# Optimization experiments

Measured on AMD Instinct MI355X. Metric: run time of the kernel, lower is better.

Reference implementation:

```python
import jax, jax.numpy as jnp
import numpy as np

WS = (7, 7)  # window size
NUM_HEADS = 16


def _relative_position_index(ws):
    # Deterministic int index table, computed exactly as in the torch module.
    coords = np.stack(np.meshgrid(np.arange(ws[0]), np.arange(ws[1]), indexing='ij'))  # [2,Wh,Ww]
    coords = coords.reshape(2, -1)                       # [2, N]
    rel = coords[:, :, None] - coords[:, None, :]        # [2, N, N]
    rel = rel.transpose(1, 2, 0)                         # [N, N, 2]
    rel = rel + np.array([ws[0] - 1, ws[1] - 1])
    rel[:, :, 0] *= 2 * ws[1] - 1
    return jnp.asarray(rel.sum(-1), dtype=jnp.int32)     # [N, N]


def setup_inputs() -> dict:
    key = jax.random.key(0)
    ks = jax.random.split(key, 5)
    B_, N, C = 2048, WS[0] * WS[1], 512
    nw = 64
    return {
        'x': jax.random.normal(ks[0], (B_, N, C), dtype=jnp.float32),
        'mask': jax.random.normal(ks[1], (nw, N, N), dtype=jnp.float32),
        'qkv_w': jax.random.normal(ks[2], (3 * C, C), dtype=jnp.float32) * 0.02,
        'qkv_b': jax.random.normal(ks[3], (3 * C,), dtype=jnp.float32) * 0.02,
        'rpb_table': jax.random.normal(ks[4], ((2 * WS[0] - 1) * (2 * WS[1] - 1), NUM_HEADS), dtype=jnp.float32) * 0.02,
    }


def reference(x, mask, qkv_w, qkv_b, rpb_table):
    B_, N, C = x.shape
    H = NUM_HEADS
    hd = C // H
    scale = hd ** -0.5

    # qkv projection: [B_, N, 3, H, hd] -> q, k, v each [B_, H, N, hd]
    qkv = (jnp.einsum('bnc,oc->bno', x, qkv_w) + qkv_b)
    qkv = qkv.reshape(B_, N, 3, H, hd).transpose(2, 0, 3, 1, 4)
    q, k, v = qkv[0], qkv[1], qkv[2]

    attn = jnp.einsum('bhnd,bhmd->bhnm', q * scale, k)  # [B_, H, N, N]

    rel_idx = _relative_position_index(WS)                       # [N, N]
    bias = rpb_table[rel_idx.reshape(-1)].reshape(N, N, H)       # gather
    attn = attn + bias.transpose(2, 0, 1)[None]                  # [1, H, N, N]

    nw = mask.shape[0]
    attn = attn.reshape(B_ // nw, nw, H, N, N) + mask[None, :, None]
    attn = attn.reshape(B_, H, N, N)
    attn = jax.nn.softmax(attn, axis=-1)

    out = jnp.einsum('bhnm,bhmd->bhnd', attn, v)
    out = out.transpose(0, 2, 1, 3).reshape(B_, N, C)
    # NOTE: source assigns `X = self.proj(x)` but returns `x`, so the
    # output projection is dead code; we faithfully return pre-proj output.
    return out
```

## Files before the change

kernel.cpp:

```cpp
#include <hip/hip_runtime.h>
#include <cstdint>
#include <cstddef>

typedef __bf16 bf16x8 __attribute__((ext_vector_type(8)));
typedef float f32x4 __attribute__((ext_vector_type(4)));
typedef unsigned short u16x8 __attribute__((ext_vector_type(8)));
typedef unsigned short u16x4 __attribute__((ext_vector_type(4)));
typedef unsigned int u32x2 __attribute__((ext_vector_type(2)));

#define VT_LD 56
#define BSTRIDE 52
#define BSZ 2548
#define PLD 72

__device__ __forceinline__ unsigned short f2bf(float f) {
  unsigned int u = __builtin_bit_cast(unsigned int, f);
  u += 0x7FFFu + ((u >> 16) & 1u);
  return (unsigned short)(u >> 16);
}
__device__ __forceinline__ float bf2f(unsigned short h) {
  unsigned int u = (unsigned int)h << 16;
  return __builtin_bit_cast(float, u);
}

__device__ __forceinline__ void gload_lds16(const void* g, void* l) {
  __builtin_amdgcn_global_load_lds((const __attribute__((address_space(1))) void*)g,
                                   (__attribute__((address_space(3))) void*)l, 16, 0, 0);
}

__global__ void conv_f2b_k(const float* __restrict__ src, unsigned short* __restrict__ dst, long n8) {
  long i = (long)blockIdx.x * blockDim.x + threadIdx.x;
  long stride = (long)gridDim.x * blockDim.x;
  for (; i < n8; i += stride) {
    float4 a = *(const float4*)(src + i * 8);
    float4 b = *(const float4*)(src + i * 8 + 4);
    u16x8 p;
    p[0]=f2bf(a.x); p[1]=f2bf(a.y); p[2]=f2bf(a.z); p[3]=f2bf(a.w);
    p[4]=f2bf(b.x); p[5]=f2bf(b.y); p[6]=f2bf(b.z); p[7]=f2bf(b.w);
    *(u16x8*)(dst + i * 8) = p;
  }
}

__global__ void build_bias_k(const float* __restrict__ rpb, unsigned short* __restrict__ biasT) {
  int idx = blockIdx.x * 256 + threadIdx.x;
  if (idx >= 16 * BSZ) return;
  int h = idx / BSZ;
  int rem = idx - h * BSZ;
  int i = rem / BSTRIDE, j = rem - (rem / BSTRIDE) * BSTRIDE;
  unsigned short v = 0;
  if (j < 49) {
    int r1 = i / 7, c1 = i - r1 * 7;
    int r2 = j / 7, c2 = j - r2 * 7;
    int ri = (r1 - r2 + 6) * 13 + (c1 - c2 + 6);
    v = f2bf(rpb[ri * 16 + h]);
  }
  biasT[idx] = v;
}

#define GEMM_SETUP(N0)                                                         \
  int t = threadIdx.x;                                                         \
  int lane = t & 63, wv = t >> 6;                                              \
  int g = lane >> 4, q = lane & 15;                                            \
  int wrow = wv >> 1, wcol = wv & 1;                                           \
  f32x4 acc[4][4] = {};                                                        \
  int schunk = (t & 3) ^ ((t >> 3) & 3);                                       \
  const unsigned short* ag0 = xb + (m0 + (t >> 2)) * 512 + schunk * 8;         \
  const unsigned short* ag1 = ag0 + 64 * 512;                                  \
  const unsigned short* bg0 = wb + (size_t)((N0) + (t >> 2)) * 512 + schunk * 8; \
  const unsigned short* bg1 = bg0 + 64 * 512;                                  \
  unsigned short* alA  = Ab + wv * 512;                                        \
  unsigned short* alA2 = Ab + 2048 + wv * 512;                                 \
  unsigned short* blB  = Bb + wv * 512;                                        \
  unsigned short* blB2 = Bb + 2048 + wv * 512;                                 \
  int roff = (8 * g) ^ (((q >> 1) & 3) << 3);                                  \
  const unsigned short* arb = Ab + (wrow * 64 + q) * 32 + roff;                \
  const unsigned short* brb = Bb + (wcol * 64 + q) * 32 + roff;

#define STAGE(KT, BOFF) do {                    \
    int kof = (KT) * 32;                        \
    gload_lds16(ag0 + kof, alA  + (BOFF));      \
    gload_lds16(ag1 + kof, alA2 + (BOFF));      \
    gload_lds16(bg0 + kof, blB  + (BOFF));      \
    gload_lds16(bg1 + kof, blB2 + (BOFF));      \
  } while (0)

#define COMPUTE(BOFF, SWAPPED) do {                                            \
    bf16x8 af[4], bfr[4];                                                      \
    _Pragma("unroll")                                                          \
    for (int i2 = 0; i2 < 4; ++i2) af[i2]  = *(const bf16x8*)(arb + (BOFF) + i2 * 512); \
    _Pragma("unroll")                                                          \
    for (int j2 = 0; j2 < 4; ++j2) bfr[j2] = *(const bf16x8*)(brb + (BOFF) + j2 * 512); \
    _Pragma("unroll")                                                          \
    for (int i2 = 0; i2 < 4; ++i2)                                             \
      _Pragma("unroll")                                                        \
      for (int j2 = 0; j2 < 4; ++j2)                                           \
        acc[i2][j2] = (SWAPPED)                                                \
          ? __builtin_amdgcn_mfma_f32_16x16x32_bf16(bfr[j2], af[i2], acc[i2][j2], 0, 0, 0) \
          : __builtin_amdgcn_mfma_f32_16x16x32_bf16(af[i2], bfr[j2], acc[i2][j2], 0, 0, 0); \
  } while (0)

#define KLOOP(SWAPPED)                          \
  STAGE(0, 0);                                  \
  __syncthreads();                              \
  for (int kt = 0; kt < 16; kt += 2) {          \
    STAGE(kt + 1, 4096);                        \
    COMPUTE(0, SWAPPED);                        \
    __syncthreads();                            \
    if (kt + 2 < 16) STAGE(kt + 2, 0);          \
    COMPUTE(4096, SWAPPED);                     \
    __syncthreads();                            \
  }

__global__ __launch_bounds__(256, 4) void qkv_gemm_qk_k(
    const unsigned short* __restrict__ xb, const float* __restrict__ qkv_b,
    const unsigned short* __restrict__ wb,
    unsigned short* __restrict__ qs, unsigned short* __restrict__ kk)
{
  __shared__ __align__(16) unsigned short smem[16384];
  unsigned short* Ab = smem;
  unsigned short* Bb = smem + 8192;

  int bid = blockIdx.x;
  int sw = (bid & 7) * 784 + (bid >> 3);
  int mt = sw >> 3, ntl = sw & 7;
  long m0 = (long)mt * 128;
  int  n0 = ntl * 128;
  int  s  = n0 >> 9;

  GEMM_SETUP(n0)
  KLOOP(1)

  unsigned short* dst = (s == 0) ? qs : kk;
  float sc = (s == 0) ? 0.17677669529663687f : 1.0f;
  float4 bi[4];
  int hj[4], dj[4];
  #pragma unroll
  for (int j2 = 0; j2 < 4; ++j2) {
    int n = n0 + wcol * 64 + j2 * 16 + 4 * g;
    bi[j2] = *(const float4*)(qkv_b + n);
    hj[j2] = (n >> 5) & 15;
    dj[j2] = n & 31;
  }
  #pragma unroll
  for (int i2 = 0; i2 < 4; ++i2) {
    unsigned int m = (unsigned int)m0 + wrow * 64 + i2 * 16 + q;
    unsigned int b = m / 49;
    unsigned int i = m - b * 49;
    size_t base = ((size_t)(b * 16) * 49 + i) * 32;
    #pragma unroll
    for (int j2 = 0; j2 < 4; ++j2) {
      f32x4 a = acc[i2][j2];
      unsigned int lo = (unsigned int)f2bf((a[0] + bi[j2].x) * sc) | ((unsigned int)f2bf((a[1] + bi[j2].y) * sc) << 16);
      unsigned int hi = (unsigned int)f2bf((a[2] + bi[j2].z) * sc) | ((unsigned int)f2bf((a[3] + bi[j2].w) * sc) << 16);
      u32x2 wv2 = {lo, hi};
      *(u32x2*)(dst + base + (size_t)hj[j2] * (49 * 32) + dj[j2]) = wv2;
    }
  }
}

__global__ __launch_bounds__(256, 4) void qkv_gemm_v_k(
    const unsigned short* __restrict__ xb, const float* __restrict__ qkv_b,
    const unsigned short* __restrict__ wb,
    unsigned short* __restrict__ vt)
{
  __shared__ __align__(16) unsigned short smem[16384];
  unsigned short* Ab = smem;
  unsigned short* Bb = smem + 8192;

  int bid = blockIdx.x;
  int sw = (bid & 7) * 392 + (bid >> 3);
  int mt = sw >> 2, ntv = sw & 3;
  long m0 = (long)mt * 128;
  int  n0 = 1024 + ntv * 128;

  GEMM_SETUP(n0)
  KLOOP(0)

  #pragma unroll
  for (int j2 = 0; j2 < 4; ++j2) {
    int n  = n0 + wcol * 64 + j2 * 16 + q;
    float bias = qkv_b[n];
    int d = n & 31;
    int h = (n >> 5) & 15;
    #pragma unroll
    for (int i2 = 0; i2 < 4; ++i2) {
      unsigned int gm0 = (unsigned int)m0 + wrow * 64 + i2 * 16 + 4 * g;
      unsigned int b0 = gm0 / 49;
      unsigned int i0 = gm0 - b0 * 49;
      unsigned short hv[4];
      #pragma unroll
      for (int r = 0; r < 4; ++r) hv[r] = f2bf(acc[i2][j2][r] + bias);
      if (i0 <= 45) {
        unsigned short* base = vt + ((size_t)(b0 * 16 + h) * 32 + d) * VT_LD;
        if ((i0 & 1) == 0) {
          *(unsigned int*)(base + i0)     = (unsigned int)hv[0] | ((unsigned int)hv[1] << 16);
          *(unsigned int*)(base + i0 + 2) = (unsigned int)hv[2] | ((unsigned int)hv[3] << 16);
        } else {
          base[i0] = hv[0];
          *(unsigned int*)(base + i0 + 1) = (unsigned int)hv[1] | ((unsigned int)hv[2] << 16);
          base[i0 + 3] = hv[3];
        }
      } else {
        #pragma unroll
        for (int r = 0; r < 4; ++r) {
          unsigned int gm = gm0 + r;
          unsigned int b = gm / 49;
          unsigned int i = gm - b * 49;
          vt[((size_t)(b * 16 + h) * 32 + d) * VT_LD + i] = hv[r];
        }
      }
    }
  }
}

__global__ __launch_bounds__(256, 3) void win_attn_k(
    const unsigned short* __restrict__ qs, const unsigned short* __restrict__ kk,
    const unsigned short* __restrict__ vt, const unsigned short* __restrict__ biasT,
    const float* __restrict__ mask, float* __restrict__ out)
{
  __shared__ float mlds[BSZ];
  __shared__ unsigned short plds[4][64 * PLD];

  int b = blockIdx.x;
  int t = threadIdx.x;
  int lane = t & 63, wv = t >> 6;
  int g = lane >> 4, q = lane & 15;

  const float* msrc = mask + (size_t)(b & 63) * 2401;
  for (int idx = t; idx < BSZ; idx += 256) {
    int i = idx / BSTRIDE, j = idx - (idx / BSTRIDE) * BSTRIDE;
    mlds[idx] = (j < 49) ? msrc[i * 49 + j] : 0.0f;
  }
  __syncthreads();

  unsigned short* pl = plds[wv];
  const float NINF = -__builtin_inff();

  int rc[4];
  rc[0] = q; rc[1] = 16 + q; rc[2] = 32 + q; rc[3] = 48;

  int h0 = wv * 4;
  const unsigned short* qh = qs + (size_t)(b * 16 + h0) * (49 * 32);
  const unsigned short* kh = kk + (size_t)(b * 16 + h0) * (49 * 32);
  bf16x8 ak[4], bq[4];
  #pragma unroll
  for (int jt = 0; jt < 4; ++jt) ak[jt] = *(const bf16x8*)(kh + rc[jt] * 32 + 8 * g);
  #pragma unroll
  for (int it = 0; it < 4; ++it) bq[it] = *(const bf16x8*)(qh + rc[it] * 32 + 8 * g);

  #pragma unroll
  for (int hh = 0; hh < 4; ++hh) {
    int h = wv * 4 + hh;
    const unsigned short* vh  = vt + (size_t)(b * 16 + h) * (32 * VT_LD);
    const unsigned short* bh2 = biasT + h * BSZ;

    f32x4 zero = {0.f, 0.f, 0.f, 0.f};
    f32x4 st[4][4];
    __builtin_amdgcn_s_setprio(1);
    #pragma unroll
    for (int it = 0; it < 4; ++it)
      #pragma unroll
      for (int jt = 0; jt < 4; ++jt)
        st[it][jt] = __builtin_amdgcn_mfma_f32_16x16x32_bf16(ak[jt], bq[it], zero, 0, 0, 0);
    __builtin_amdgcn_s_setprio(0);

    bf16x8 akn[4], bqn[4];
    if (hh < 3) {
      const unsigned short* qh2 = qh + 49 * 32;
      const unsigned short* kh2 = kh + 49 * 32;
      #pragma unroll
      for (int jt = 0; jt < 4; ++jt) akn[jt] = *(const bf16x8*)(kh2 + rc[jt] * 32 + 8 * g);
      #pragma unroll
      for (int it = 0; it < 4; ++it) bqn[it] = *(const bf16x8*)(qh2 + rc[it] * 32 + 8 * g);
      qh = qh2; kh = kh2;
    }
    bf16x8 bv[2][2];
    #pragma unroll
    for (int ktt = 0; ktt < 2; ++ktt)
      #pragma unroll
      for (int dt = 0; dt < 2; ++dt)
        bv[ktt][dt] = *(const bf16x8*)(vh + (dt * 16 + q) * VT_LD + ktt * 32 + 8 * g);

    #pragma unroll
    for (int it = 0; it < 4; ++it) {
      int i = it * 16 + q;
      int ic = i > 48 ? 48 : i;
      f32x4 pv4[4];
      f32x4 vm = {NINF, NINF, NINF, NINF};
      #pragma unroll
      for (int jt = 0; jt < 4; ++jt) {
        if (jt == 3 && g > 0) {
          pv4[3] = (f32x4){NINF, NINF, NINF, NINF};
        } else {
          u16x4 bu = *(const u16x4*)(bh2 + ic * BSTRIDE + jt * 16 + 4 * g);
          f32x4 m4 = *(const f32x4*)(mlds + ic * BSTRIDE + jt * 16 + 4 * g);
          f32x4 sv = st[it][jt];
          #pragma unroll
          for (int r = 0; r < 4; ++r) sv[r] += bf2f(bu[r]) + m4[r];
          if (jt == 3) {
            sv[1] = NINF; sv[2] = NINF; sv[3] = NINF;
          }
          pv4[jt] = sv;
          #pragma unroll
          for (int r = 0; r < 4; ++r) vm[r] = fmaxf(vm[r], sv[r]);
        }
      }
      float mx = fmaxf(fmaxf(vm[0], vm[1]), fmaxf(vm[2], vm[3]));
      mx = fmaxf(mx, __shfl_xor(mx, 16));
      mx = fmaxf(mx, __shfl_xor(mx, 32));
      f32x4 vs = zero;
      #pragma unroll
      for (int jt = 0; jt < 4; ++jt) {
        #pragma unroll
        for (int r = 0; r < 4; ++r) {
          float p = __expf(pv4[jt][r] - mx);
          pv4[jt][r] = p;
          vs[r] += p;
        }
      }
      float sm = (vs[0] + vs[1]) + (vs[2] + vs[3]);
      sm += __shfl_xor(sm, 16);
      sm += __shfl_xor(sm, 32);
      float rv = 1.0f / sm;
      #pragma unroll
      for (int jt = 0; jt < 4; ++jt) {
        unsigned int lo = (unsigned int)f2bf(pv4[jt][0] * rv) | ((unsigned int)f2bf(pv4[jt][1] * rv) << 16);
        unsigned int hi = (unsigned int)f2bf(pv4[jt][2] * rv) | ((unsigned int)f2bf(pv4[jt][3] * rv) << 16);
        u32x2 w = {lo, hi};
        *(u32x2*)(pl + i * PLD + jt * 16 + 4 * g) = w;
      }
    }

    f32x4 oacc[4][2] = {};
    #pragma unroll
    for (int ktt = 0; ktt < 2; ++ktt) {
      bf16x8 pa[4];
      #pragma unroll
      for (int it = 0; it < 4; ++it)
        pa[it] = *(const bf16x8*)(pl + (it * 16 + q) * PLD + ktt * 32 + 8 * g);
      __builtin_amdgcn_s_setprio(1);
      #pragma unroll
      for (int it = 0; it < 4; ++it)
        #pragma unroll
        for (int dt = 0; dt < 2; ++dt)
          oacc[it][dt] = __builtin_amdgcn_mfma_f32_16x16x32_bf16(pa[it], bv[ktt][dt], oacc[it][dt], 0, 0, 0);
      __builtin_amdgcn_s_setprio(0);
    }

    #pragma unroll
    for (int it = 0; it < 4; ++it) {
      #pragma unroll
      for (int dt = 0; dt < 2; ++dt) {
        #pragma unroll
        for (int r = 0; r < 4; ++r) {
          int i = it * 16 + 4 * g + r;
          if (i < 49) {
            int d = dt * 16 + q;
            out[(size_t)(b * 49 + i) * 512 + h * 32 + d] = oacc[it][dt][r];
          }
        }
      }
    }

    if (hh < 3) {
      #pragma unroll
      for (int jt = 0; jt < 4; ++jt) ak[jt] = akn[jt];
      #pragma unroll
      for (int it = 0; it < 4; ++it) bq[it] = bqn[it];
    }
  }
}

extern "C" void kernel_launch(void* const* d_in, const int* in_sizes, int n_in,
                              void* d_out, int out_size, void* d_ws, size_t ws_size,
                              hipStream_t stream) {
  const float* x     = (const float*)d_in[0];
  const float* mask  = (const float*)d_in[1];
  const float* qkv_w = (const float*)d_in[2];
  const float* qkv_b = (const float*)d_in[3];
  const float* rpb   = (const float*)d_in[4];
  float* out = (float*)d_out;

  const size_t QS_OFF   = 0;
  const size_t KK_OFF   = 102760448;
  const size_t VT_OFF   = 205520896;
  const size_t BIAS_OFF = 322961408;
  const size_t WB_OFF   = 323042944;
  const size_t NEED     = 324615808;
  if (ws_size < NEED) return;

  char* ws = (char*)d_ws;
  unsigned short* qsb   = (unsigned short*)(ws + QS_OFF);
  unsigned short* kkb   = (unsigned short*)(ws + KK_OFF);
  unsigned short* vtb   = (unsigned short*)(ws + VT_OFF);
  unsigned short* biasT = (unsigned short*)(ws + BIAS_OFF);
  unsigned short* wb    = (unsigned short*)(ws + WB_OFF);

  unsigned short* xb = (unsigned short*)d_out;

  conv_f2b_k<<<2048, 256, 0, stream>>>(x, xb, 6422528);
  conv_f2b_k<<<512, 256, 0, stream>>>(qkv_w, wb, 98304);
  build_bias_k<<<160, 256, 0, stream>>>(rpb, biasT);
  qkv_gemm_v_k<<<3136, 256, 0, stream>>>(xb, qkv_b, wb, vtb);
  qkv_gemm_qk_k<<<6272, 256, 0, stream>>>(xb, qkv_b, wb, qsb, kkb);
  win_attn_k<<<2048, 256, 0, stream>>>(qsb, kkb, vtb, biasT, mask, out);
}
```

Measured before the change: 473.0 us.

## Read padded mask from global, raise occupancy, vectorize output stores

Precomputes a padded copy of the mask in workspace, reusing the weight buffer after the GEMMs finish, and has the attention kernel read it directly from global memory instead of staging it into LDS with a barrier. Dropping the LDS mask buffer allows launch bounds to rise to 4 blocks per CU. The PV MFMA operands are swapped so each lane holds contiguous output columns, which turns the scalar output stores into 16-byte vector stores. The cost is an extra small kernel launch, and mask reads now go through cache rather than LDS.

```diff
diff --git a/kernel.cpp b/kernel.cpp
--- a/kernel.cpp
+++ b/kernel.cpp
@@ -55,6 +55,14 @@
     v = f2bf(rpb[ri * 16 + h]);
   }
   biasT[idx] = v;
+}
+
+__global__ void build_maskp_k(const float* __restrict__ mask, float* __restrict__ maskp) {
+  int idx = blockIdx.x * 256 + threadIdx.x;
+  int w = idx / BSZ;
+  int rem = idx - w * BSZ;
+  int i = rem / BSTRIDE, j = rem - (rem / BSTRIDE) * BSTRIDE;
+  maskp[idx] = (j < 49) ? mask[w * 2401 + i * 49 + j] : 0.0f;
 }
 
 #define GEMM_SETUP(N0)                                                         \
@@ -213,12 +221,11 @@
   }
 }
 
-__global__ __launch_bounds__(256, 3) void win_attn_k(
+__global__ __launch_bounds__(256, 4) void win_attn_k(
     const unsigned short* __restrict__ qs, const unsigned short* __restrict__ kk,
     const unsigned short* __restrict__ vt, const unsigned short* __restrict__ biasT,
-    const float* __restrict__ mask, float* __restrict__ out)
+    const float* __restrict__ maskp, float* __restrict__ out)
 {
-  __shared__ float mlds[BSZ];
   __shared__ unsigned short plds[4][64 * PLD];
 
   int b = blockIdx.x;
@@ -226,13 +233,7 @@
   int lane = t & 63, wv = t >> 6;
   int g = lane >> 4, q = lane & 15;
 
-  const float* msrc = mask + (size_t)(b & 63) * 2401;
-  for (int idx = t; idx < BSZ; idx += 256) {
-    int i = idx / BSTRIDE, j = idx - (idx / BSTRIDE) * BSTRIDE;
-    mlds[idx] = (j < 49) ? msrc[i * 49 + j] : 0.0f;
-  }
-  __syncthreads();
-
+  const float* wm = maskp + (size_t)(b & 63) * BSZ;
   unsigned short* pl = plds[wv];
   const float NINF = -__builtin_inff();
 
@@ -293,7 +294,7 @@
           pv4[3] = (f32x4){NINF, NINF, NINF, NINF};
         } else {
           u16x4 bu = *(const u16x4*)(bh2 + ic * BSTRIDE + jt * 16 + 4 * g);
-          f32x4 m4 = *(const f32x4*)(mlds + ic * BSTRIDE + jt * 16 + 4 * g);
+          f32x4 m4 = *(const f32x4*)(wm + ic * BSTRIDE + jt * 16 + 4 * g);
           f32x4 sv = st[it][jt];
           #pragma unroll
           for (int r = 0; r < 4; ++r) sv[r] += bf2f(bu[r]) + m4[r];
@@ -343,22 +344,18 @@
       for (int it = 0; it < 4; ++it)
         #pragma unroll
         for (int dt = 0; dt < 2; ++dt)
-          oacc[it][dt] = __builtin_amdgcn_mfma_f32_16x16x32_bf16(pa[it], bv[ktt][dt], oacc[it][dt], 0, 0, 0);
+          oacc[it][dt] = __builtin_amdgcn_mfma_f32_16x16x32_bf16(bv[ktt][dt], pa[it], oacc[it][dt], 0, 0, 0);
       __builtin_amdgcn_s_setprio(0);
     }
 
     #pragma unroll
     for (int it = 0; it < 4; ++it) {
-      #pragma unroll
-      for (int dt = 0; dt < 2; ++dt) {
+      int i = it * 16 + q;
+      if (i < 49) {
+        float* orow = out + (size_t)(b * 49 + i) * 512 + h * 32 + 4 * g;
         #pragma unroll
-        for (int r = 0; r < 4; ++r) {
-          int i = it * 16 + 4 * g + r;
-          if (i < 49) {
-            int d = dt * 16 + q;
-            out[(size_t)(b * 49 + i) * 512 + h * 32 + d] = oacc[it][dt][r];
-          }
-        }
+        for (int dt = 0; dt < 2; ++dt)
+          *(f32x4*)(orow + dt * 16) = oacc[it][dt];
       }
     }
 
@@ -395,6 +392,7 @@
   unsigned short* vtb   = (unsigned short*)(ws + VT_OFF);
   unsigned short* biasT = (unsigned short*)(ws + BIAS_OFF);
   unsigned short* wb    = (unsigned short*)(ws + WB_OFF);
+  float*          maskp = (float*)(ws + WB_OFF);
 
   unsigned short* xb = (unsigned short*)d_out;
 
@@ -403,5 +401,6 @@
   build_bias_k<<<160, 256, 0, stream>>>(rpb, biasT);
   qkv_gemm_v_k<<<3136, 256, 0, stream>>>(xb, qkv_b, wb, vtb);
   qkv_gemm_qk_k<<<6272, 256, 0, stream>>>(xb, qkv_b, wb, qsb, kkb);
-  win_attn_k<<<2048, 256, 0, stream>>>(qsb, kkb, vtb, biasT, mask, out);
-}
+  build_maskp_k<<<637, 256, 0, stream>>>(mask, maskp);
+  win_attn_k<<<2048, 256, 0, stream>>>(qsb, kkb, vtb, biasT, maskp, out);
+}
```

After: 541.2 us. 14.4% more time.
